# Kernel optimization log

Measured on AMD Instinct MI355X. Metric: run time of the kernel, lower is better.

## Reference

```python
import jax, jax.numpy as jnp
import numpy as np

SEQ_LEN = 4096
INPUT_SIZE = 1024
OUTPUT_SIZE = 1024


def _xavier(key, shape):
    n = shape[0]
    lim = 1.0 / (n ** 0.5)
    return jax.random.uniform(key, shape, minval=-lim, maxval=lim, dtype=jnp.float32)


def setup_inputs() -> dict:
    key = jax.random.key(0)
    kx, kk, kv, kq = jax.random.split(key, 4)
    X = jax.random.normal(kx, (SEQ_LEN, INPUT_SIZE), dtype=jnp.float32)
    Wk = _xavier(kk, (INPUT_SIZE, OUTPUT_SIZE))
    Wv = _xavier(kv, (INPUT_SIZE, OUTPUT_SIZE))
    Wq = _xavier(kq, (INPUT_SIZE, OUTPUT_SIZE))
    return {"X": X, "Wk": Wk, "Wv": Wv, "Wq": Wq}


def reference(X, Wk, Wv, Wq):
    # Faithful to original: scores = K @ Q^T (note K first, no 1/sqrt(d) scaling)
    K = X @ Wk  # (S, D)
    V = X @ Wv  # (S, D)
    Q = X @ Wq  # (S, D)
    scores = jnp.einsum('sd,td->st', K, Q)  # (S, S) == K @ Q^T
    attn = jax.nn.softmax(scores, axis=-1) @ V  # (S, D)
    return attn
```

## Files before the change

### kernel.cpp

```cpp
#include <hip/hip_runtime.h>
#include <hip/hip_fp16.h>
#include <cstdint>

#define SEQ 4096
#define DIM 1024

typedef _Float16 f16x8 __attribute__((ext_vector_type(8)));
typedef float f32x16 __attribute__((ext_vector_type(16)));
typedef __attribute__((address_space(1))) void as1_void;
typedef __attribute__((address_space(3))) void as3_void;

__device__ __forceinline__ ushort f2h(float f) {
  _Float16 h = (_Float16)f;
  return __builtin_bit_cast(ushort, h);
}

__global__ void convert_all_kernel(const float* __restrict__ X, const float* __restrict__ Wk,
                                   const float* __restrict__ Wv, const float* __restrict__ Wq,
                                   ushort* __restrict__ Xh, ushort* __restrict__ Wt) {
  const int z = blockIdx.z;
  const int tx = threadIdx.x, ty = threadIdx.y;
  if (z == 3) {
    const int bid = blockIdx.y * 32 + blockIdx.x;
    const int t = ty * 32 + tx;
#pragma unroll
    for (int k = 0; k < 4; k++) {
      int i = bid * 1024 + k * 256 + t;
      float4 v = reinterpret_cast<const float4*>(X)[i];
      ushort4 o = { f2h(v.x), f2h(v.y), f2h(v.z), f2h(v.w) };
      reinterpret_cast<ushort4*>(Xh)[i] = o;
    }
    return;
  }
  __shared__ float tile[32][33];
  const float* W = (z == 0) ? Wk : (z == 1) ? Wv : Wq;
  int n0 = blockIdx.x * 32, k0 = blockIdx.y * 32;
#pragma unroll
  for (int r = 0; r < 4; r++) {
    int k = ty + r * 8;
    tile[k][tx] = W[(size_t)(k0 + k) * DIM + n0 + tx];
  }
  __syncthreads();
  ushort* out = Wt + (size_t)z * DIM * DIM;
#pragma unroll
  for (int r = 0; r < 4; r++) {
    int n = ty + r * 8;
    out[(size_t)(n0 + n) * DIM + k0 + tx] = f2h(tile[tx][n]);
  }
}

__device__ __forceinline__ void gemm_tile256(const ushort* __restrict__ A,
                                             const ushort* __restrict__ B,
                                             ushort* __restrict__ C,
                                             int N, int K, int m0, int n0,
                                             int kt0, int ktend) {
  constexpr int BK = 64;
  __shared__ __align__(16) ushort As[2][256 * BK];
  __shared__ __align__(16) ushort Bs[2][256 * BK];
  const int tid = threadIdx.x;
  const int wave = tid >> 6, lane = tid & 63;
  const int l31 = lane & 31, khalf = lane >> 5;
  const int wm = (wave & 1) * 128, wn = (wave >> 1) * 64;

  const int srow = tid >> 3;
  const int skey = ((srow & 7) ^ ((srow >> 3) & 3));
  const int sce = (((tid & 7) ^ skey) * 8);
  const int rk = (l31 & 7) ^ ((l31 >> 3) & 3);

  f32x16 acc[4][2];
#pragma unroll
  for (int i = 0; i < 4; i++)
#pragma unroll
    for (int j = 0; j < 2; j++)
#pragma unroll
      for (int r = 0; r < 16; r++) acc[i][j][r] = 0.f;

  const ushort* Abase = A + (size_t)(m0 + srow) * K + sce;
  const ushort* Bbase = B + (size_t)(n0 + srow) * K + sce;
  const int ldsbase = wave * 512;

#pragma unroll
  for (int q = 0; q < 4; q++)
    __builtin_amdgcn_global_load_lds((const as1_void*)(Abase + (size_t)q * 64 * K + kt0),
                                     (as3_void*)&As[0][ldsbase + q * 4096], 16, 0, 0);
#pragma unroll
  for (int q = 0; q < 4; q++)
    __builtin_amdgcn_global_load_lds((const as1_void*)(Bbase + (size_t)q * 64 * K + kt0),
                                     (as3_void*)&Bs[0][ldsbase + q * 4096], 16, 0, 0);
  __syncthreads();

  const int ntiles = (ktend - kt0) >> 6;
  for (int tt = 0; tt < ntiles; ++tt) {
    const int cur = tt & 1;
    const int kt = kt0 + tt * BK;
    const bool pf = (tt + 1 < ntiles);
    const ushort* As_c = As[cur];
    const ushort* Bs_c = Bs[cur];
#pragma unroll
    for (int ks = 0; ks < 4; ks++) {
      f16x8 af[4], bf2[2];
      const int co = (((ks * 2 + khalf) ^ rk) * 8);
#pragma unroll
      for (int i = 0; i < 4; i++)
        af[i] = *reinterpret_cast<const f16x8*>(&As_c[(wm + i * 32 + l31) * BK + co]);
#pragma unroll
      for (int j = 0; j < 2; j++)
        bf2[j] = *reinterpret_cast<const f16x8*>(&Bs_c[(wn + j * 32 + l31) * BK + co]);
      if (pf && ks == 0) {
#pragma unroll
        for (int q = 0; q < 4; q++)
          __builtin_amdgcn_global_load_lds(
              (const as1_void*)(Abase + (size_t)q * 64 * K + kt + BK),
              (as3_void*)&As[cur ^ 1][ldsbase + q * 4096], 16, 0, 0);
      }
      if (pf && ks == 1) {
#pragma unroll
        for (int q = 0; q < 4; q++)
          __builtin_amdgcn_global_load_lds(
              (const as1_void*)(Bbase + (size_t)q * 64 * K + kt + BK),
              (as3_void*)&Bs[cur ^ 1][ldsbase + q * 4096], 16, 0, 0);
      }
      __builtin_amdgcn_s_barrier();
      __builtin_amdgcn_s_setprio(1);
#pragma unroll
      for (int i = 0; i < 4; i++)
#pragma unroll
        for (int j = 0; j < 2; j++)
          acc[i][j] = __builtin_amdgcn_mfma_f32_32x32x16_f16(af[i], bf2[j], acc[i][j], 0, 0, 0);
      __builtin_amdgcn_s_setprio(0);
      if (ks < 3) __builtin_amdgcn_s_barrier();
    }
    __syncthreads();
  }

#pragma unroll
  for (int i = 0; i < 4; i++)
#pragma unroll
    for (int j = 0; j < 2; j++)
#pragma unroll
      for (int r = 0; r < 16; r++) {
        int row = m0 + wm + i * 32 + (r & 3) + 8 * (r >> 2) + 4 * khalf;
        int col = n0 + wn + j * 32 + l31;
        C[(size_t)row * N + col] = f2h(acc[i][j][r]);
      }
}

__global__ __launch_bounds__(512, 2) void proj256_kernel(const ushort* __restrict__ Xh,
                                                         const ushort* __restrict__ Wt,
                                                         ushort* __restrict__ Kh,
                                                         ushort* __restrict__ Qh,
                                                         ushort* __restrict__ Vt) {
  const int b = blockIdx.x;
  const ushort* A;
  const ushort* B;
  ushort* Cp;
  int N, m0, n0;
  if (b < 128) {
    const int z = b >> 6, q = b & 63;
    A = Xh;
    B = Wt + (size_t)(z ? 2 : 0) * DIM * DIM;
    Cp = z ? Qh : Kh;
    N = DIM;
    m0 = (q >> 2) * 256;
    n0 = (q & 3) * 256;
  } else {
    const int q = b - 128;
    A = Wt + (size_t)DIM * DIM;
    B = Xh;
    Cp = Vt;
    N = SEQ;
    m0 = (q >> 4) * 256;
    n0 = (q & 15) * 256;
  }
  gemm_tile256(A, B, Cp, N, DIM, m0, n0, 0, DIM);
}

__global__ __launch_bounds__(512, 2) void score256_kernel(const ushort* __restrict__ Kh,
                                                          const ushort* __restrict__ Qh,
                                                          ushort* __restrict__ S) {
  const int f = blockIdx.x;
  const int t = (f & 7) * 32 + (f >> 3);
  gemm_tile256(Kh, Qh, S, SEQ, DIM, (t >> 4) * 256, (t & 15) * 256, 0, DIM);
}

__global__ __launch_bounds__(512, 2) void out256_kernel(const ushort* __restrict__ P,
                                                        const ushort* __restrict__ Vt,
                                                        ushort* __restrict__ Part) {
  const int f = blockIdx.x;
  const int z = f >> 6;
  const int q = f & 63;
  const int t = (q & 7) * 8 + (q >> 3);
  ushort* Cp = Part + (size_t)z * SEQ * DIM;
  gemm_tile256(P, Vt, Cp, DIM, SEQ, (t >> 2) * 256, (t & 3) * 256,
               z * (SEQ / 4), (z + 1) * (SEQ / 4));
}

__global__ void reduce4_kernel(const ushort* __restrict__ Part, float* __restrict__ out, int n8) {
  int i = blockIdx.x * blockDim.x + threadIdx.x;
  if (i >= n8) return;
  const f16x8* p0 = reinterpret_cast<const f16x8*>(Part);
  const f16x8* p1 = p0 + n8;
  const f16x8* p2 = p1 + n8;
  const f16x8* p3 = p2 + n8;
  f16x8 a = p0[i], b = p1[i], c = p2[i], d = p3[i];
  float4 lo, hi;
  lo.x = (float)a[0] + (float)b[0] + (float)c[0] + (float)d[0];
  lo.y = (float)a[1] + (float)b[1] + (float)c[1] + (float)d[1];
  lo.z = (float)a[2] + (float)b[2] + (float)c[2] + (float)d[2];
  lo.w = (float)a[3] + (float)b[3] + (float)c[3] + (float)d[3];
  hi.x = (float)a[4] + (float)b[4] + (float)c[4] + (float)d[4];
  hi.y = (float)a[5] + (float)b[5] + (float)c[5] + (float)d[5];
  hi.z = (float)a[6] + (float)b[6] + (float)c[6] + (float)d[6];
  hi.w = (float)a[7] + (float)b[7] + (float)c[7] + (float)d[7];
  reinterpret_cast<float4*>(out)[i * 2] = lo;
  reinterpret_cast<float4*>(out)[i * 2 + 1] = hi;
}

__global__ __launch_bounds__(256) void softmax_kernel(const ushort* __restrict__ S,
                                                      ushort* __restrict__ P) {
  const int wave = threadIdx.x >> 6, lane = threadIdx.x & 63;
  const int row = blockIdx.x * 4 + wave;
  const ushort* s = S + (size_t)row * SEQ;
  float v[64];
#pragma unroll
  for (int i = 0; i < 8; i++) {
    f16x8 h = reinterpret_cast<const f16x8*>(s)[i * 64 + lane];
#pragma unroll
    for (int j = 0; j < 8; j++) v[i * 8 + j] = (float)h[j];
  }
  float m = v[0];
#pragma unroll
  for (int j = 1; j < 64; j++) m = fmaxf(m, v[j]);
#pragma unroll
  for (int o = 32; o > 0; o >>= 1) m = fmaxf(m, __shfl_xor(m, o, 64));
  float sum = 0.f;
#pragma unroll
  for (int j = 0; j < 64; j++) {
    v[j] = __expf(v[j] - m);
    sum += v[j];
  }
#pragma unroll
  for (int o = 32; o > 0; o >>= 1) sum += __shfl_xor(sum, o, 64);
  float inv = 1.0f / sum;
  ushort* p = P + (size_t)row * SEQ;
#pragma unroll
  for (int i = 0; i < 8; i++) {
    f16x8 h;
#pragma unroll
    for (int j = 0; j < 8; j++) h[j] = (_Float16)(v[i * 8 + j] * inv);
    reinterpret_cast<f16x8*>(p)[i * 64 + lane] = h;
  }
}

extern "C" void kernel_launch(void* const* d_in, const int* in_sizes, int n_in,
                              void* d_out, int out_size, void* d_ws, size_t ws_size,
                              hipStream_t stream) {
  const float* X = (const float*)d_in[0];
  const float* Wk = (const float*)d_in[1];
  const float* Wv = (const float*)d_in[2];
  const float* Wq = (const float*)d_in[3];

  char* ws = (char*)d_ws;
  size_t off = 0;
  ushort* Xh = (ushort*)(ws + off); off += (size_t)SEQ * DIM * 2;
  ushort* Wt = (ushort*)(ws + off); off += (size_t)3 * DIM * DIM * 2;
  ushort* Kh = (ushort*)(ws + off); off += (size_t)SEQ * DIM * 2;
  ushort* Qh = (ushort*)(ws + off); off += (size_t)SEQ * DIM * 2;
  ushort* Vt = (ushort*)(ws + off); off += (size_t)SEQ * DIM * 2;
  ushort* S = (ushort*)(ws + off);  off += (size_t)SEQ * SEQ * 2;
  ushort* P = (ushort*)(ws + off);  off += (size_t)SEQ * SEQ * 2;

  ushort* Part = S;

  convert_all_kernel<<<dim3(32, 32, 4), dim3(32, 8), 0, stream>>>(X, Wk, Wv, Wq, Xh, Wt);
  proj256_kernel<<<256, 512, 0, stream>>>(Xh, Wt, Kh, Qh, Vt);
  score256_kernel<<<256, 512, 0, stream>>>(Kh, Qh, S);
  softmax_kernel<<<1024, 256, 0, stream>>>(S, P);
  out256_kernel<<<256, 512, 0, stream>>>(P, Vt, Part);
  reduce4_kernel<<<SEQ * DIM / 8 / 256, 256, 0, stream>>>(Part, (float*)d_out, SEQ * DIM / 8);
}
```

Before: 208.1 us.

## Fuse all attention stages into one cooperative persistent kernel with grid syncs

Replaces the six separate launches (convert, projection, score GEMM, softmax, PV GEMM, reduce) with a single cooperative kernel of 256 blocks. Stages are separated by grid.sync() and share one 128KB LDS buffer. The goal is to remove per-launch overhead and inter-kernel gaps. In exchange, occupancy drops to one block per CU, where the old kernels ran two, and the light elementwise stages lose parallelism. The projection stage also leaves 64 blocks idle.

```diff
diff --git a/kernel.cpp b/kernel.cpp
--- a/kernel.cpp
+++ b/kernel.cpp
@@ -1,6 +1,9 @@
 #include <hip/hip_runtime.h>
 #include <hip/hip_fp16.h>
+#include <hip/hip_cooperative_groups.h>
 #include <cstdint>
+
+namespace cg = cooperative_groups;
 
 #define SEQ 4096
 #define DIM 1024
@@ -15,48 +18,15 @@
   return __builtin_bit_cast(ushort, h);
 }
 
-__global__ void convert_all_kernel(const float* __restrict__ X, const float* __restrict__ Wk,
-                                   const float* __restrict__ Wv, const float* __restrict__ Wq,
-                                   ushort* __restrict__ Xh, ushort* __restrict__ Wt) {
-  const int z = blockIdx.z;
-  const int tx = threadIdx.x, ty = threadIdx.y;
-  if (z == 3) {
-    const int bid = blockIdx.y * 32 + blockIdx.x;
-    const int t = ty * 32 + tx;
-#pragma unroll
-    for (int k = 0; k < 4; k++) {
-      int i = bid * 1024 + k * 256 + t;
-      float4 v = reinterpret_cast<const float4*>(X)[i];
-      ushort4 o = { f2h(v.x), f2h(v.y), f2h(v.z), f2h(v.w) };
-      reinterpret_cast<ushort4*>(Xh)[i] = o;
-    }
-    return;
-  }
-  __shared__ float tile[32][33];
-  const float* W = (z == 0) ? Wk : (z == 1) ? Wv : Wq;
-  int n0 = blockIdx.x * 32, k0 = blockIdx.y * 32;
-#pragma unroll
-  for (int r = 0; r < 4; r++) {
-    int k = ty + r * 8;
-    tile[k][tx] = W[(size_t)(k0 + k) * DIM + n0 + tx];
-  }
-  __syncthreads();
-  ushort* out = Wt + (size_t)z * DIM * DIM;
-#pragma unroll
-  for (int r = 0; r < 4; r++) {
-    int n = ty + r * 8;
-    out[(size_t)(n0 + n) * DIM + k0 + tx] = f2h(tile[tx][n]);
-  }
-}
-
-__device__ __forceinline__ void gemm_tile256(const ushort* __restrict__ A,
-                                             const ushort* __restrict__ B,
-                                             ushort* __restrict__ C,
-                                             int N, int K, int m0, int n0,
-                                             int kt0, int ktend) {
+__device__ __forceinline__ void gemm256(ushort* __restrict__ sm,
+                                        const ushort* __restrict__ A,
+                                        const ushort* __restrict__ B,
+                                        ushort* __restrict__ C,
+                                        int N, int K, int m0, int n0,
+                                        int kt0, int ktend) {
   constexpr int BK = 64;
-  __shared__ __align__(16) ushort As[2][256 * BK];
-  __shared__ __align__(16) ushort Bs[2][256 * BK];
+  ushort* AsB[2] = { sm, sm + 16384 };
+  ushort* BsB[2] = { sm + 32768, sm + 49152 };
   const int tid = threadIdx.x;
   const int wave = tid >> 6, lane = tid & 63;
   const int l31 = lane & 31, khalf = lane >> 5;
@@ -79,27 +49,28 @@
   const ushort* Bbase = B + (size_t)(n0 + srow) * K + sce;
   const int ldsbase = wave * 512;
 
+  const int ntiles = (ktend - kt0) >> 6;
+
 #pragma unroll
   for (int q = 0; q < 4; q++)
     __builtin_amdgcn_global_load_lds((const as1_void*)(Abase + (size_t)q * 64 * K + kt0),
-                                     (as3_void*)&As[0][ldsbase + q * 4096], 16, 0, 0);
+                                     (as3_void*)&AsB[0][ldsbase + q * 4096], 16, 0, 0);
 #pragma unroll
   for (int q = 0; q < 4; q++)
     __builtin_amdgcn_global_load_lds((const as1_void*)(Bbase + (size_t)q * 64 * K + kt0),
-                                     (as3_void*)&Bs[0][ldsbase + q * 4096], 16, 0, 0);
+                                     (as3_void*)&BsB[0][ldsbase + q * 4096], 16, 0, 0);
   __syncthreads();
 
-  const int ntiles = (ktend - kt0) >> 6;
   for (int tt = 0; tt < ntiles; ++tt) {
-    const int cur = tt & 1;
-    const int kt = kt0 + tt * BK;
+    const int cur = tt & 1, nb = cur ^ 1;
+    const int nkt = kt0 + (tt + 1) * BK;
     const bool pf = (tt + 1 < ntiles);
-    const ushort* As_c = As[cur];
-    const ushort* Bs_c = Bs[cur];
+    const ushort* As_c = AsB[cur];
+    const ushort* Bs_c = BsB[cur];
 #pragma unroll
     for (int ks = 0; ks < 4; ks++) {
       f16x8 af[4], bf2[2];
-      const int co = (((ks * 2 + khalf) ^ rk) * 8);
+      const int co = (((ks * 2 + khalf)) ^ rk) * 8;
 #pragma unroll
       for (int i = 0; i < 4; i++)
         af[i] = *reinterpret_cast<const f16x8*>(&As_c[(wm + i * 32 + l31) * BK + co]);
@@ -109,16 +80,14 @@
       if (pf && ks == 0) {
 #pragma unroll
         for (int q = 0; q < 4; q++)
-          __builtin_amdgcn_global_load_lds(
-              (const as1_void*)(Abase + (size_t)q * 64 * K + kt + BK),
-              (as3_void*)&As[cur ^ 1][ldsbase + q * 4096], 16, 0, 0);
+          __builtin_amdgcn_global_load_lds((const as1_void*)(Abase + (size_t)q * 64 * K + nkt),
+                                           (as3_void*)&AsB[nb][ldsbase + q * 4096], 16, 0, 0);
       }
       if (pf && ks == 1) {
 #pragma unroll
         for (int q = 0; q < 4; q++)
-          __builtin_amdgcn_global_load_lds(
-              (const as1_void*)(Bbase + (size_t)q * 64 * K + kt + BK),
-              (as3_void*)&Bs[cur ^ 1][ldsbase + q * 4096], 16, 0, 0);
+          __builtin_amdgcn_global_load_lds((const as1_void*)(Bbase + (size_t)q * 64 * K + nkt),
+                                           (as3_void*)&BsB[nb][ldsbase + q * 4096], 16, 0, 0);
       }
       __builtin_amdgcn_s_barrier();
       __builtin_amdgcn_s_setprio(1);
@@ -145,110 +114,146 @@
       }
 }
 
-__global__ __launch_bounds__(512, 2) void proj256_kernel(const ushort* __restrict__ Xh,
-                                                         const ushort* __restrict__ Wt,
-                                                         ushort* __restrict__ Kh,
-                                                         ushort* __restrict__ Qh,
-                                                         ushort* __restrict__ Vt) {
-  const int b = blockIdx.x;
-  const ushort* A;
-  const ushort* B;
-  ushort* Cp;
-  int N, m0, n0;
-  if (b < 128) {
-    const int z = b >> 6, q = b & 63;
-    A = Xh;
-    B = Wt + (size_t)(z ? 2 : 0) * DIM * DIM;
-    Cp = z ? Qh : Kh;
-    N = DIM;
-    m0 = (q >> 2) * 256;
-    n0 = (q & 3) * 256;
-  } else {
-    const int q = b - 128;
-    A = Wt + (size_t)DIM * DIM;
-    B = Xh;
-    Cp = Vt;
-    N = SEQ;
-    m0 = (q >> 4) * 256;
-    n0 = (q & 15) * 256;
-  }
-  gemm_tile256(A, B, Cp, N, DIM, m0, n0, 0, DIM);
-}
-
-__global__ __launch_bounds__(512, 2) void score256_kernel(const ushort* __restrict__ Kh,
-                                                          const ushort* __restrict__ Qh,
-                                                          ushort* __restrict__ S) {
-  const int f = blockIdx.x;
-  const int t = (f & 7) * 32 + (f >> 3);
-  gemm_tile256(Kh, Qh, S, SEQ, DIM, (t >> 4) * 256, (t & 15) * 256, 0, DIM);
-}
-
-__global__ __launch_bounds__(512, 2) void out256_kernel(const ushort* __restrict__ P,
-                                                        const ushort* __restrict__ Vt,
-                                                        ushort* __restrict__ Part) {
-  const int f = blockIdx.x;
-  const int z = f >> 6;
-  const int q = f & 63;
-  const int t = (q & 7) * 8 + (q >> 3);
-  ushort* Cp = Part + (size_t)z * SEQ * DIM;
-  gemm_tile256(P, Vt, Cp, DIM, SEQ, (t >> 2) * 256, (t & 3) * 256,
-               z * (SEQ / 4), (z + 1) * (SEQ / 4));
-}
-
-__global__ void reduce4_kernel(const ushort* __restrict__ Part, float* __restrict__ out, int n8) {
-  int i = blockIdx.x * blockDim.x + threadIdx.x;
-  if (i >= n8) return;
-  const f16x8* p0 = reinterpret_cast<const f16x8*>(Part);
-  const f16x8* p1 = p0 + n8;
-  const f16x8* p2 = p1 + n8;
-  const f16x8* p3 = p2 + n8;
-  f16x8 a = p0[i], b = p1[i], c = p2[i], d = p3[i];
-  float4 lo, hi;
-  lo.x = (float)a[0] + (float)b[0] + (float)c[0] + (float)d[0];
-  lo.y = (float)a[1] + (float)b[1] + (float)c[1] + (float)d[1];
-  lo.z = (float)a[2] + (float)b[2] + (float)c[2] + (float)d[2];
-  lo.w = (float)a[3] + (float)b[3] + (float)c[3] + (float)d[3];
-  hi.x = (float)a[4] + (float)b[4] + (float)c[4] + (float)d[4];
-  hi.y = (float)a[5] + (float)b[5] + (float)c[5] + (float)d[5];
-  hi.z = (float)a[6] + (float)b[6] + (float)c[6] + (float)d[6];
-  hi.w = (float)a[7] + (float)b[7] + (float)c[7] + (float)d[7];
-  reinterpret_cast<float4*>(out)[i * 2] = lo;
-  reinterpret_cast<float4*>(out)[i * 2 + 1] = hi;
-}
-
-__global__ __launch_bounds__(256) void softmax_kernel(const ushort* __restrict__ S,
-                                                      ushort* __restrict__ P) {
-  const int wave = threadIdx.x >> 6, lane = threadIdx.x & 63;
-  const int row = blockIdx.x * 4 + wave;
-  const ushort* s = S + (size_t)row * SEQ;
-  float v[64];
-#pragma unroll
-  for (int i = 0; i < 8; i++) {
-    f16x8 h = reinterpret_cast<const f16x8*>(s)[i * 64 + lane];
-#pragma unroll
-    for (int j = 0; j < 8; j++) v[i * 8 + j] = (float)h[j];
-  }
-  float m = v[0];
-#pragma unroll
-  for (int j = 1; j < 64; j++) m = fmaxf(m, v[j]);
-#pragma unroll
-  for (int o = 32; o > 0; o >>= 1) m = fmaxf(m, __shfl_xor(m, o, 64));
-  float sum = 0.f;
-#pragma unroll
-  for (int j = 0; j < 64; j++) {
-    v[j] = __expf(v[j] - m);
-    sum += v[j];
-  }
-#pragma unroll
-  for (int o = 32; o > 0; o >>= 1) sum += __shfl_xor(sum, o, 64);
-  float inv = 1.0f / sum;
-  ushort* p = P + (size_t)row * SEQ;
-#pragma unroll
-  for (int i = 0; i < 8; i++) {
-    f16x8 h;
-#pragma unroll
-    for (int j = 0; j < 8; j++) h[j] = (_Float16)(v[i * 8 + j] * inv);
-    reinterpret_cast<f16x8*>(p)[i * 64 + lane] = h;
+__global__ __launch_bounds__(512, 1) void fused_attn_kernel(
+    const float* __restrict__ X, const float* __restrict__ Wk,
+    const float* __restrict__ Wv, const float* __restrict__ Wq,
+    ushort* __restrict__ Xh, ushort* __restrict__ Wt,
+    ushort* __restrict__ Kh, ushort* __restrict__ Qh, ushort* __restrict__ Vt,
+    ushort* __restrict__ S, ushort* __restrict__ P, float* __restrict__ O) {
+  __shared__ __align__(16) ushort smem[65536];
+  cg::grid_group grid = cg::this_grid();
+  const int bid = blockIdx.x;
+  const int tid = threadIdx.x;
+
+  {
+#pragma unroll
+    for (int it = 0; it < 8; it++) {
+      int i = it * 131072 + bid * 512 + tid;
+      float4 v = reinterpret_cast<const float4*>(X)[i];
+      ushort4 o = { f2h(v.x), f2h(v.y), f2h(v.z), f2h(v.w) };
+      reinterpret_cast<ushort4*>(Xh)[i] = o;
+    }
+    float* tile = reinterpret_cast<float*>(smem);
+    const int g = tid >> 8;
+    const int t256 = tid & 255;
+    const int ttx = t256 & 31, tty = t256 >> 5;
+    float* tl = tile + g * (32 * 33);
+#pragma unroll
+    for (int it = 0; it < 6; it++) {
+      int tileid = bid * 12 + it * 2 + g;
+      int z = tileid >> 10;
+      int rem = tileid & 1023;
+      int n0 = (rem & 31) * 32, k0 = (rem >> 5) * 32;
+      const float* W = (z == 0) ? Wk : (z == 1) ? Wv : Wq;
+#pragma unroll
+      for (int r = 0; r < 4; r++) {
+        int k = tty + r * 8;
+        tl[k * 33 + ttx] = W[(size_t)(k0 + k) * DIM + n0 + ttx];
+      }
+      __syncthreads();
+      ushort* outp = Wt + (size_t)z * DIM * DIM;
+#pragma unroll
+      for (int r = 0; r < 4; r++) {
+        int n = tty + r * 8;
+        outp[(size_t)(n0 + n) * DIM + k0 + ttx] = f2h(tl[ttx * 33 + n]);
+      }
+      __syncthreads();
+    }
+  }
+  grid.sync();
+
+  if (bid < 192) {
+    if (bid < 64) {
+      gemm256(smem, Xh, Wt, Kh, DIM, DIM, (bid >> 2) * 256, (bid & 3) * 256, 0, DIM);
+    } else if (bid < 128) {
+      const int q = bid - 64;
+      gemm256(smem, Xh, Wt + (size_t)2 * DIM * DIM, Qh, DIM, DIM,
+              (q >> 2) * 256, (q & 3) * 256, 0, DIM);
+    } else {
+      const int q = bid - 128;
+      gemm256(smem, Wt + (size_t)DIM * DIM, Xh, Vt, SEQ, DIM,
+              (q >> 4) * 256, (q & 15) * 256, 0, DIM);
+    }
+  }
+  grid.sync();
+
+  {
+    const int t = (bid & 7) * 32 + (bid >> 3);
+    gemm256(smem, Kh, Qh, S, SEQ, DIM, (t >> 4) * 256, (t & 15) * 256, 0, DIM);
+  }
+  grid.sync();
+
+  {
+    const int wv = tid >> 6, ln = tid & 63;
+#pragma unroll
+    for (int rr = 0; rr < 2; rr++) {
+      const int row = bid * 16 + wv * 2 + rr;
+      const ushort* s = S + (size_t)row * SEQ;
+      float v[64];
+#pragma unroll
+      for (int i = 0; i < 8; i++) {
+        f16x8 h = reinterpret_cast<const f16x8*>(s)[i * 64 + ln];
+#pragma unroll
+        for (int j = 0; j < 8; j++) v[i * 8 + j] = (float)h[j];
+      }
+      float m = v[0];
+#pragma unroll
+      for (int j = 1; j < 64; j++) m = fmaxf(m, v[j]);
+#pragma unroll
+      for (int o = 32; o > 0; o >>= 1) m = fmaxf(m, __shfl_xor(m, o, 64));
+      float sum = 0.f;
+#pragma unroll
+      for (int j = 0; j < 64; j++) {
+        v[j] = __expf(v[j] - m);
+        sum += v[j];
+      }
+#pragma unroll
+      for (int o = 32; o > 0; o >>= 1) sum += __shfl_xor(sum, o, 64);
+      float inv = 1.0f / sum;
+      ushort* p = P + (size_t)row * SEQ;
+#pragma unroll
+      for (int i = 0; i < 8; i++) {
+        f16x8 h;
+#pragma unroll
+        for (int j = 0; j < 8; j++) h[j] = (_Float16)(v[i * 8 + j] * inv);
+        reinterpret_cast<f16x8*>(p)[i * 64 + ln] = h;
+      }
+    }
+  }
+  grid.sync();
+
+  {
+    const int z = bid >> 6;
+    const int q = bid & 63;
+    const int t = (q & 7) * 8 + (q >> 3);
+    ushort* Part = S + (size_t)z * SEQ * DIM;
+    gemm256(smem, P, Vt, Part, DIM, SEQ, (t >> 2) * 256, (t & 3) * 256,
+            z * (SEQ / 4), (z + 1) * (SEQ / 4));
+  }
+  grid.sync();
+
+  {
+    const int n8 = SEQ * DIM / 8;
+    const f16x8* p0 = reinterpret_cast<const f16x8*>(S);
+    const f16x8* p1 = p0 + n8;
+    const f16x8* p2 = p1 + n8;
+    const f16x8* p3 = p2 + n8;
+#pragma unroll
+    for (int it = 0; it < 4; it++) {
+      int i = it * 131072 + bid * 512 + tid;
+      f16x8 a = p0[i], b = p1[i], c = p2[i], d = p3[i];
+      float4 lo, hi;
+      lo.x = (float)a[0] + (float)b[0] + (float)c[0] + (float)d[0];
+      lo.y = (float)a[1] + (float)b[1] + (float)c[1] + (float)d[1];
+      lo.z = (float)a[2] + (float)b[2] + (float)c[2] + (float)d[2];
+      lo.w = (float)a[3] + (float)b[3] + (float)c[3] + (float)d[3];
+      hi.x = (float)a[4] + (float)b[4] + (float)c[4] + (float)d[4];
+      hi.y = (float)a[5] + (float)b[5] + (float)c[5] + (float)d[5];
+      hi.z = (float)a[6] + (float)b[6] + (float)c[6] + (float)d[6];
+      hi.w = (float)a[7] + (float)b[7] + (float)c[7] + (float)d[7];
+      reinterpret_cast<float4*>(O)[i * 2] = lo;
+      reinterpret_cast<float4*>(O)[i * 2 + 1] = hi;
+    }
   }
 }
 
@@ -267,15 +272,13 @@
   ushort* Kh = (ushort*)(ws + off); off += (size_t)SEQ * DIM * 2;
   ushort* Qh = (ushort*)(ws + off); off += (size_t)SEQ * DIM * 2;
   ushort* Vt = (ushort*)(ws + off); off += (size_t)SEQ * DIM * 2;
-  ushort* S = (ushort*)(ws + off);  off += (size_t)SEQ * SEQ * 2;
-  ushort* P = (ushort*)(ws + off);  off += (size_t)SEQ * SEQ * 2;
-
-  ushort* Part = S;
-
-  convert_all_kernel<<<dim3(32, 32, 4), dim3(32, 8), 0, stream>>>(X, Wk, Wv, Wq, Xh, Wt);
-  proj256_kernel<<<256, 512, 0, stream>>>(Xh, Wt, Kh, Qh, Vt);
-  score256_kernel<<<256, 512, 0, stream>>>(Kh, Qh, S);
-  softmax_kernel<<<1024, 256, 0, stream>>>(S, P);
-  out256_kernel<<<256, 512, 0, stream>>>(P, Vt, Part);
-  reduce4_kernel<<<SEQ * DIM / 8 / 256, 256, 0, stream>>>(Part, (float*)d_out, SEQ * DIM / 8);
-}
+  ushort* S  = (ushort*)(ws + off); off += (size_t)SEQ * SEQ * 2;
+  ushort* P  = (ushort*)(ws + off); off += (size_t)SEQ * SEQ * 2;
+  float* O = (float*)d_out;
+
+  void* args[] = { (void*)&X, (void*)&Wk, (void*)&Wv, (void*)&Wq,
+                   (void*)&Xh, (void*)&Wt, (void*)&Kh, (void*)&Qh, (void*)&Vt,
+                   (void*)&S, (void*)&P, (void*)&O };
+  hipLaunchCooperativeKernel((const void*)fused_attn_kernel,
+                             dim3(256), dim3(512), args, 0, stream);
+}
```

After: 426.3 us. 2.05x slower.
